# Optimization experiments

Hardware: AMD Instinct MI355X
Metric: run time of the kernel (lower is better)

The kernel has to match this reference:

```python
import jax, jax.numpy as jnp
import numpy as np

N_NODES = 50000
N_EDGES = 1200000
N_REL = 45
IN_C, HID_C, OUT_C = 64, 32, 16


def setup_inputs() -> dict:
    key = jax.random.key(0)
    ks = jax.random.split(key, 9)
    x = jax.random.normal(ks[0], (N_NODES, IN_C), dtype=jnp.float32)
    edge_index = jax.random.randint(ks[1], (2, N_EDGES), 0, N_NODES, dtype=jnp.int64)
    edge_type = jax.random.randint(ks[2], (N_EDGES,), 0, N_REL, dtype=jnp.int64)
    s = 0.05
    W1 = jax.random.normal(ks[3], (N_REL, IN_C, HID_C), dtype=jnp.float32) * s
    root1 = jax.random.normal(ks[4], (IN_C, HID_C), dtype=jnp.float32) * s
    b1 = jax.random.normal(ks[5], (HID_C,), dtype=jnp.float32) * s
    W2 = jax.random.normal(ks[6], (N_REL, HID_C, OUT_C), dtype=jnp.float32) * s
    root2 = jax.random.normal(ks[7], (HID_C, OUT_C), dtype=jnp.float32) * s
    b2 = jax.random.normal(ks[8], (OUT_C,), dtype=jnp.float32) * s
    return {"x": x, "edge_index": edge_index, "edge_type": edge_type,
            "W1": W1, "root1": root1, "b1": b1,
            "W2": W2, "root2": root2, "b2": b2}


def rgcn_conv(x, edge_index, edge_type, W, root, b):
    # PyG RGCNConv: out_i = x_i @ root + b + sum_r mean_{j in N_r(i)} (x_j @ W_r)
    N = x.shape[0]
    R = W.shape[0]
    src, dst = edge_index[0], edge_index[1]
    # per-relation transform of all nodes: [R, N, out]
    h = jnp.einsum('ni,rio->rno', x, W)
    # per-edge message: gather transformed src feature for edge's relation
    msg = h[edge_type, src]                      # [E, out]
    # segment id combines (relation, dst) for per-relation mean aggregation
    seg = edge_type * N + dst                    # [E]
    sums = jax.ops.segment_sum(msg, seg, num_segments=R * N)        # [R*N, out]
    cnt = jax.ops.segment_sum(jnp.ones((msg.shape[0],), x.dtype), seg,
                              num_segments=R * N)                   # [R*N]
    mean = sums / jnp.maximum(cnt, 1.0)[:, None]
    agg = mean.reshape(R, N, -1).sum(axis=0)     # sum over relations -> [N, out]
    return agg + x @ root + b


def reference(x, edge_index, edge_type, W1, root1, b1, W2, root2, b2):
    h = rgcn_conv(x, edge_index, edge_type, W1, root1, b1)
    h = jax.nn.relu(h)
    out = rgcn_conv(h, edge_index, edge_type, W2, root2, b2)
    return out
```

## Files before the change

kernel.cpp:

```cpp
#include <hip/hip_runtime.h>
#include <hip/hip_fp16.h>
#include <cstdint>
#include <cstddef>

#define NN   50000
#define NE   1200000
#define NR   45
#define INC  64
#define HIDC 32
#define OUTC 16
#define MAXE 1202880
#define NCHUNK (MAXE/64)
#define EPB 4096
#define NB  ((NE + EPB - 1) / EPB)
#define QDW2 12500
#define QDD2 25000
#define NTILE ((NN + 255) / 256)


typedef _Float16 f16x8 __attribute__((ext_vector_type(8)));
typedef float    f32x4 __attribute__((ext_vector_type(4)));

union F16Bits { unsigned short u; _Float16 f; };
union ABFrag   { uint4 u; f16x8 f; };

__global__ __launch_bounds__(256) void preph_k(const float* __restrict__ W1,
                                               const float* __restrict__ W2,
                                               const float* __restrict__ x,
                                               const int* __restrict__ ei,
                                               const int* __restrict__ et,
                                               __half* __restrict__ W1f,
                                               __half* __restrict__ W2f,
                                               __half* __restrict__ xh,
                                               unsigned* __restrict__ ghist,
                                               unsigned* __restrict__ rsorted,
                                               unsigned* __restrict__ flagbuf) {
    __shared__ unsigned lh[NR];
    int t = threadIdx.x, b = blockIdx.x;
    if (t < NR) lh[t] = 0;
    __syncthreads();
    if (b < NB) {
        #pragma unroll
        for (int it = 0; it < EPB / 256; ++it) {
            int e = b * EPB + it * 256 + t;
            if (e < NE) {
                int r = et[e], src = ei[e], dst = ei[NE + e];
                if ((unsigned)r < NR && (unsigned)src < NN && (unsigned)dst < NN)
                    atomicAdd(&lh[r], 1u);
            }
        }
    }
    __syncthreads();
    if (b < NB && t < NR) ghist[b * NR + t] = lh[t];
    int g = b * 256 + t;
    int gthreads = gridDim.x * 256;
    for (int i = g; i < MAXE; i += gthreads) rsorted[i] = 0xFFFFFFFFu;
    if (b == 0) flagbuf[t] = 0;
    if (g < NR * 2048) {
        int r = g >> 11, rem = g & 2047;
        int kb = rem >> 10, nb = (rem >> 9) & 1;
        int lane = (rem >> 3) & 63, j = rem & 7;
        int k = kb * 32 + (lane >> 4) * 8 + j;
        int n = nb * 16 + (lane & 15);
        W1f[g] = __float2half(W1[(r * INC + k) * HIDC + n]);
    }
    if (g < NR * 512) {
        int r = g >> 9, rem = g & 511;
        int lane = (rem >> 3) & 63, j = rem & 7;
        int k = (lane >> 4) * 8 + j;
        int kc = (k >> 1) + ((k & 1) << 4);
        int n = lane & 15;
        W2f[g] = __float2half(W2[(r * HIDC + kc) * OUTC + n]);
    }
    if (g < NN * INC / 2) {
        float2 f = ((const float2*)x)[g];
        union { __half2 h; unsigned u; } cv;
        cv.h = __floats2half2_rn(f.x, f.y);
        ((unsigned*)xh)[g] = cv.u;
    }
}

__global__ __launch_bounds__(1024) void scat_k(const int* __restrict__ ei,
                                               const int* __restrict__ et,
                                               const unsigned* __restrict__ ghist,
                                               unsigned* __restrict__ rngs,
                                               int* __restrict__ chunkrel,
                                               unsigned* __restrict__ rsorted) {
    __shared__ unsigned reltot[NR];
    __shared__ unsigned mypart[NR];
    __shared__ unsigned relbase[NR + 1];
    __shared__ unsigned lbase[NR], lcur[NR];
    int t = threadIdx.x, bx = blockIdx.x;
    if (t < NR) {
        unsigned total = 0, part = 0;
        for (int b = 0; b < NB; ++b) {
            if (b == bx) part = total;
            total += ghist[b * NR + t];
        }
        reltot[t] = total;
        mypart[t] = part;
        lcur[t] = 0;
    }
    __syncthreads();
    if (t == 0) {
        unsigned acc = 0;
        for (int r = 0; r < NR; ++r) {
            relbase[r] = acc;
            acc += ((reltot[r] + 63u) >> 6) << 6;
        }
        relbase[NR] = acc;
    }
    __syncthreads();
    if (t < NR) lbase[t] = relbase[t] + mypart[t];
    __syncthreads();
    #pragma unroll
    for (int it = 0; it < EPB / 1024; ++it) {
        int e = bx * EPB + it * 1024 + t;
        if (e < NE) {
            int r = et[e], src = ei[e], dst = ei[NE + e];
            if ((unsigned)r < NR && (unsigned)src < NN && (unsigned)dst < NN) {
                unsigned local = atomicAdd(&lcur[r], 1u);
                rsorted[lbase[r] + local] = (unsigned)src | ((unsigned)dst << 16);
            }
        }
    }
    if (bx == 0) {
        if (t < NR) {
            rngs[2 * t]     = relbase[t];
            rngs[2 * t + 1] = relbase[t] + reltot[t];
        }
        for (int c = t; c < NCHUNK; c += 1024) {
            unsigned pos = (unsigned)c << 6;
            int lo = 0, hi = NR - 1;
            while (lo < hi) {
                int mid = (lo + hi + 1) >> 1;
                if (relbase[mid] <= pos) lo = mid; else hi = mid - 1;
            }
            chunkrel[c] = lo;
        }
    }
}

__global__ __launch_bounds__(1024) void relcnt_k(const unsigned* __restrict__ rsorted,
                                                 const unsigned* __restrict__ rngs,
                                                 unsigned short* __restrict__ cnt16,
                                                 unsigned short* __restrict__ rank16) {
    __shared__ unsigned lds[QDW2];
    int r = blockIdx.x >> 1, q = blockIdx.x & 1, t = threadIdx.x;
    unsigned base = rngs[2 * r], end = rngs[2 * r + 1];
    unsigned dlo = q * QDD2, dhi = dlo + QDD2;
    for (int w = t; w < QDW2; w += 1024) lds[w] = 0;
    __syncthreads();
    for (unsigned s = base + t; s < end; s += 1024) {
        unsigned d = rsorted[s] >> 16;
        if (d >= dlo && d < dhi) {
            unsigned off = d - dlo;
            unsigned old = atomicAdd(&lds[off >> 1], (off & 1) ? 0x10000u : 1u);
            rank16[s] = (unsigned short)((off & 1) ? (old >> 16) : (old & 0xFFFFu));
        }
    }
    __syncthreads();
    unsigned* __restrict__ cp = (unsigned*)(cnt16 + (size_t)r * NN + dlo);
    for (int w = t; w < QDW2; w += 1024) cp[w] = lds[w];
}

__global__ __launch_bounds__(256) void dp_k(const unsigned short* __restrict__ cnt16,
                                            unsigned* __restrict__ packed,
                                            unsigned* __restrict__ rowptr,
                                            unsigned* __restrict__ flags) {
    __shared__ unsigned wsum[4];
    __shared__ unsigned excl_s;
    int t = threadIdx.x, b = blockIdx.x;
    int lane = t & 63, wv = t >> 6;
    int dst = b * 256 + t;
    unsigned deg = 0;
    if (dst < NN) {
        unsigned run = 0;
        #pragma unroll 5
        for (int r = 0; r < NR; ++r) {
            unsigned c = cnt16[(size_t)r * NN + dst];
            F16Bits fb; fb.f = (_Float16)(c ? 1.0f / (float)c : 0.0f);
            packed[(size_t)r * NN + dst] = (run & 0xFFFFu) | ((unsigned)fb.u << 16);
            run += c;
        }
        deg = run;
    }
    unsigned s = deg;
    #pragma unroll
    for (int off = 1; off < 64; off <<= 1) {
        unsigned n = __shfl_up(s, off);
        if (lane >= off) s += n;
    }
    if (lane == 63) wsum[wv] = s;
    __syncthreads();
    unsigned waveoff = 0;
    if (wv > 0) waveoff += wsum[0];
    if (wv > 1) waveoff += wsum[1];
    if (wv > 2) waveoff += wsum[2];
    unsigned blockT = wsum[0] + wsum[1] + wsum[2] + wsum[3];
    unsigned local_excl = waveoff + s - deg;
    if (t == 0) {
        if (b == 0) {
            excl_s = 0;
            atomicExch(&flags[0], 0x80000000u | blockT);
        } else {
            atomicExch(&flags[b], 0x40000000u | blockT);
            unsigned ex = 0;
            int p = b - 1;
            while (p >= 0) {
                unsigned f = atomicAdd(&flags[p], 0u);
                unsigned st = f >> 30;
                if (st == 0) continue;
                ex += f & 0x3FFFFFFFu;
                if (st >= 2) break;
                --p;
            }
            excl_s = ex;
            atomicExch(&flags[b], 0x80000000u | (ex + blockT));
        }
    }
    __syncthreads();
    unsigned ex = excl_s;
    if (dst < NN) rowptr[dst] = ex + local_excl;
    if (b == (int)gridDim.x - 1 && t == 0) rowptr[NN] = ex + blockT;
}

__global__ __launch_bounds__(256) void finalize_k(const unsigned* __restrict__ rsorted,
                                                  const unsigned short* __restrict__ rank16,
                                                  const unsigned* __restrict__ packed,
                                                  const unsigned* __restrict__ rowptr,
                                                  const int* __restrict__ chunkrel,
                                                  uint2* __restrict__ pedges) {
    int s = blockIdx.x * 256 + threadIdx.x;
    if (s >= MAXE) return;
    unsigned v = rsorted[s];
    unsigned dst = v >> 16;
    if (dst >= NN) { pedges[s] = make_uint2(0u, 0x80000000u); return; }
    int r = chunkrel[s >> 6];
    unsigned pk = packed[(size_t)r * NN + dst];
    unsigned dpos = rowptr[dst] + (pk & 0xFFFFu) + (unsigned)rank16[s];
    pedges[s] = make_uint2((v & 0xFFFFu) | (pk & 0xFFFF0000u),
                           dpos | ((unsigned)r << 25));
}

__global__ __launch_bounds__(256) void msg1_k(const __half* __restrict__ xh,
                                              const __half* __restrict__ W1f,
                                              const uint2* __restrict__ pedges,
                                              __half* __restrict__ msg) {
    int tid = threadIdx.x;
    int lane = tid & 63;
    int wave = (blockIdx.x * 256 + tid) >> 6;
    if (wave >= NCHUNK) return;
    int e = (wave << 6) + lane;
    uint2 er = pedges[e];
    int w1 = (int)er.y;
    int rel = __builtin_amdgcn_readfirstlane((w1 >> 25) & 63);
    F16Bits fb; fb.u = (unsigned short)(er.x >> 16);
    float sc = (float)fb.f;
    int src = er.x & 0xFFFF;
    int drow = (w1 < 0) ? NE : (w1 & 0x1FFFFFF);
    const uint4* __restrict__ wf = (const uint4*)W1f + (size_t)rel * 256;
    ABFrag b00, b01, b10, b11;
    b00.u = wf[0 * 64 + lane];
    b01.u = wf[1 * 64 + lane];
    b10.u = wf[2 * 64 + lane];
    b11.u = wf[3 * 64 + lane];
    int quad = lane >> 4, col = lane & 15;
    ABFrag a0[4], a1[4];
    #pragma unroll
    for (int tl = 0; tl < 4; ++tl) {
        int s = __shfl(src, tl * 16 + col);
        const uint4* __restrict__ xp = (const uint4*)(xh + (size_t)s * INC) + quad;
        a0[tl].u = xp[0];
        a1[tl].u = xp[4];
    }
    #pragma unroll
    for (int tl = 0; tl < 4; ++tl) {
        f32x4 acc0 = {0.f, 0.f, 0.f, 0.f}, acc1 = {0.f, 0.f, 0.f, 0.f};
        acc0 = __builtin_amdgcn_mfma_f32_16x16x32_f16(a0[tl].f, b00.f, acc0, 0, 0, 0);
        acc0 = __builtin_amdgcn_mfma_f32_16x16x32_f16(a1[tl].f, b10.f, acc0, 0, 0, 0);
        acc1 = __builtin_amdgcn_mfma_f32_16x16x32_f16(a0[tl].f, b01.f, acc1, 0, 0, 0);
        acc1 = __builtin_amdgcn_mfma_f32_16x16x32_f16(a1[tl].f, b11.f, acc1, 0, 0, 0);
        #pragma unroll
        for (int i = 0; i < 4; ++i) {
            int ee = tl * 16 + quad * 4 + i;
            int dr   = __shfl(drow, ee);
            float si = __shfl(sc, ee);
            union { __half2 h; unsigned u; } cv;
            cv.h = __floats2half2_rn(acc0[i] * si, acc1[i] * si);
            ((unsigned*)(msg + (size_t)dr * HIDC))[col] = cv.u;
        }
    }
}

__global__ __launch_bounds__(256) void msg2_k(const __half* __restrict__ hh,
                                              const __half* __restrict__ W2f,
                                              const uint2* __restrict__ pedges,
                                              __half* __restrict__ msg) {
    int tid = threadIdx.x;
    int lane = tid & 63;
    int wave = (blockIdx.x * 256 + tid) >> 6;
    if (wave >= NCHUNK) return;
    int e = (wave << 6) + lane;
    uint2 er = pedges[e];
    int w1 = (int)er.y;
    int rel = __builtin_amdgcn_readfirstlane((w1 >> 25) & 63);
    F16Bits fb; fb.u = (unsigned short)(er.x >> 16);
    float sc = (float)fb.f;
    int src = er.x & 0xFFFF;
    int drow = (w1 < 0) ? NE : (w1 & 0x1FFFFFF);
    ABFrag bf;
    bf.u = ((const uint4*)W2f + (size_t)rel * 64)[lane];
    int quad = lane >> 4, col = lane & 15;
    ABFrag a[4];
    #pragma unroll
    for (int tl = 0; tl < 4; ++tl) {
        int s = __shfl(src, tl * 16 + col);
        a[tl].u = *((const uint4*)(hh + (size_t)s * HIDC) + quad);
    }
    #pragma unroll
    for (int tl = 0; tl < 4; ++tl) {
        f32x4 acc = {0.f, 0.f, 0.f, 0.f};
        acc = __builtin_amdgcn_mfma_f32_16x16x32_f16(a[tl].f, bf.f, acc, 0, 0, 0);
        #pragma unroll
        for (int i = 0; i < 4; ++i) {
            int ee = tl * 16 + quad * 4 + i;
            int dr   = __shfl(drow, ee);
            float si = __shfl(sc, ee);
            float v  = acc[i] * si;
            float p  = __shfl_xor(v, 8);
            if (col < 8) {
                union { __half2 h; unsigned u; } cv;
                cv.h = __floats2half2_rn(v, p);
                ((unsigned*)(msg + (size_t)dr * OUTC))[col] = cv.u;
            }
        }
    }
}

__global__ __launch_bounds__(256) void gather1_k(const float* __restrict__ x,
                                                 const float* __restrict__ root1,
                                                 const float* __restrict__ b1,
                                                 const __half* __restrict__ msg,
                                                 const unsigned* __restrict__ rowptr,
                                                 __half* __restrict__ hh) {
    __shared__ float sr[INC * HIDC];
    for (int k = threadIdx.x; k < INC * HIDC; k += 256) sr[k] = root1[k];
    __syncthreads();
    int wid = (blockIdx.x * 256 + threadIdx.x) >> 6;
    int lane = threadIdx.x & 63;
    int c2 = lane & 15, sub = lane >> 4;
    unsigned k0 = rowptr[wid], k1 = rowptr[wid + 1];
    float accx = 0.f, accy = 0.f;
    for (unsigned k = k0 + sub; k < k1; k += 4) {
        union { __half2 hh2; unsigned u; } cv;
        cv.u = ((const unsigned*)(msg + (size_t)k * HIDC))[c2];
        float2 f = __half22float2(cv.hh2);
        accx += f.x; accy += f.y;
    }
    const float4* __restrict__ xp = (const float4*)(x + (size_t)wid * INC + sub * 16);
    #pragma unroll
    for (int q = 0; q < 4; ++q) {
        float4 xr = xp[q];
        const float* xs = (const float*)&xr;
        #pragma unroll
        for (int j = 0; j < 4; ++j) {
            int in = sub * 16 + q * 4 + j;
            accx = fmaf(xs[j], sr[in * HIDC + c2], accx);
            accy = fmaf(xs[j], sr[in * HIDC + c2 + 16], accy);
        }
    }
    accx += __shfl_xor(accx, 16); accy += __shfl_xor(accy, 16);
    accx += __shfl_xor(accx, 32); accy += __shfl_xor(accy, 32);
    if (sub == 0) {
        float vx = accx + b1[c2], vy = accy + b1[c2 + 16];
        union { __half2 h2; unsigned u; } cv;
        cv.h2 = __floats2half2_rn(vx > 0.f ? vx : 0.f, vy > 0.f ? vy : 0.f);
        ((unsigned*)hh)[(size_t)wid * (HIDC / 2) + c2] = cv.u;
    }
}

__global__ __launch_bounds__(256) void gather2_k(const __half* __restrict__ hh,
                                                 const float* __restrict__ root2,
                                                 const float* __restrict__ b2,
                                                 const __half* __restrict__ msg,
                                                 const unsigned* __restrict__ rowptr,
                                                 float* __restrict__ out) {
    __shared__ float sr[HIDC * OUTC];
    for (int k = threadIdx.x; k < HIDC * OUTC; k += 256) sr[k] = root2[k];
    __syncthreads();
    int wid = (blockIdx.x * 256 + threadIdx.x) >> 6;
    int lane = threadIdx.x & 63;
    int c2 = lane & 7, sub = lane >> 3;
    unsigned k0 = rowptr[wid], k1 = rowptr[wid + 1];
    float accx = 0.f, accy = 0.f;
    for (unsigned k = k0 + sub; k < k1; k += 8) {
        union { __half2 hh2; unsigned u; } cv;
        cv.u = ((const unsigned*)(msg + (size_t)k * OUTC))[c2];
        float2 f = __half22float2(cv.hh2);
        accx += f.x; accy += f.y;
    }
    uint2 hw = *(const uint2*)(hh + (size_t)wid * HIDC + sub * 4);
    union { __half2 h2; unsigned u; } ca, cb;
    ca.u = hw.x; cb.u = hw.y;
    float2 ha = __half22float2(ca.h2), hb = __half22float2(cb.h2);
    float hs[4] = { ha.x, ha.y, hb.x, hb.y };
    #pragma unroll
    for (int j = 0; j < 4; ++j) {
        int in = 2 * sub + (j >> 1) + ((j & 1) << 4);
        accx = fmaf(hs[j], sr[in * OUTC + c2], accx);
        accy = fmaf(hs[j], sr[in * OUTC + c2 + 8], accy);
    }
    accx += __shfl_xor(accx, 8);  accy += __shfl_xor(accy, 8);
    accx += __shfl_xor(accx, 16); accy += __shfl_xor(accy, 16);
    accx += __shfl_xor(accx, 32); accy += __shfl_xor(accy, 32);
    if (sub == 0) {
        out[(size_t)wid * OUTC + c2]     = accx + b2[c2];
        out[(size_t)wid * OUTC + c2 + 8] = accy + b2[c2 + 8];
    }
}

extern "C" void kernel_launch(void* const* d_in, const int* in_sizes, int n_in,
                              void* d_out, int out_size, void* d_ws, size_t ws_size,
                              hipStream_t stream) {
    const float* x     = (const float*)d_in[0];
    const int*   ei    = (const int*)d_in[1];
    const int*   et    = (const int*)d_in[2];
    const float* W1    = (const float*)d_in[3];
    const float* root1 = (const float*)d_in[4];
    const float* b1    = (const float*)d_in[5];
    const float* W2    = (const float*)d_in[6];
    const float* root2 = (const float*)d_in[7];
    const float* b2    = (const float*)d_in[8];
    float* out = (float*)d_out;

    char* ws = (char*)d_ws;
    size_t o = 0;
    auto alloc = [&](size_t bytes) -> char* {
        char* p = ws + o;
        o = (o + bytes + 255) & ~(size_t)255;
        return p;
    };
    unsigned* rsorted = (unsigned*)alloc((size_t)MAXE * 4);
    unsigned* flagbuf = (unsigned*)alloc(256 * 4);
    unsigned* ghist   = (unsigned*)alloc((size_t)NR * NB * 4);
    unsigned* rngs    = (unsigned*)alloc((size_t)NR * 2 * 4);
    int*      chunkrel= (int*)     alloc((size_t)NCHUNK * 4);
    unsigned short* rank16 = (unsigned short*)alloc((size_t)MAXE * 2);
    unsigned short* cnt16  = (unsigned short*)alloc((size_t)NR * NN * 2);
    unsigned* packed  = (unsigned*)alloc((size_t)NR * NN * 4);
    unsigned* rowptr  = (unsigned*)alloc(((size_t)NN + 1) * 4);
    uint2*    pedges  = (uint2*)   alloc((size_t)MAXE * 8);
    __half*   W1f     = (__half*)  alloc((size_t)NR * 2048 * 2);
    __half*   W2f     = (__half*)  alloc((size_t)NR * 512 * 2);
    __half*   xh      = (__half*)  alloc((size_t)NN * INC * 2);
    __half*   hh      = (__half*)  alloc((size_t)NN * HIDC * 2);
    char*     msgraw  = alloc(((size_t)NE + 1) * 64);
    __half*   msg1    = (__half*)msgraw;
    __half*   msg2    = (__half*)msgraw;

    int prep_grid = NN * INC / 2 / 256;
    preph_k   <<<prep_grid, 256, 0, stream>>>(W1, W2, x, ei, et, W1f, W2f, xh,
                                              ghist, rsorted, flagbuf);
    scat_k    <<<NB, 1024, 0, stream>>>(ei, et, ghist, rngs, chunkrel, rsorted);
    relcnt_k  <<<2 * NR, 1024, 0, stream>>>(rsorted, rngs, cnt16, rank16);
    dp_k      <<<NTILE, 256, 0, stream>>>(cnt16, packed, rowptr, flagbuf + 32);
    finalize_k<<<(MAXE + 255) / 256, 256, 0, stream>>>(rsorted, rank16, packed,
                                                       rowptr, chunkrel, pedges);
    msg1_k    <<<(MAXE + 255) / 256, 256, 0, stream>>>(xh, W1f, pedges, msg1);
    gather1_k <<<NN * 64 / 256, 256, 0, stream>>>(x, root1, b1, msg1, rowptr, hh);
    msg2_k    <<<(MAXE + 255) / 256, 256, 0, stream>>>(hh, W2f, pedges, msg2);
    gather2_k <<<NN * 64 / 256, 256, 0, stream>>>(hh, root2, b2, msg2, rowptr, out);
}
```

Baseline: 296.8 us.

## Privatize histograms, transpose ghist, split relcnt finer, add nontemporal hints, fp16 root input

```diff
diff --git a/kernel.cpp b/kernel.cpp
--- a/kernel.cpp
+++ b/kernel.cpp
@@ -13,8 +13,8 @@
 #define NCHUNK (MAXE/64)
 #define EPB 4096
 #define NB  ((NE + EPB - 1) / EPB)
-#define QDW2 12500
-#define QDD2 25000
+#define QDW 6250
+#define QDD 12500
 #define NTILE ((NN + 255) / 256)
 
 
@@ -35,9 +35,10 @@
                                                unsigned* __restrict__ ghist,
                                                unsigned* __restrict__ rsorted,
                                                unsigned* __restrict__ flagbuf) {
-    __shared__ unsigned lh[NR];
+    __shared__ unsigned lh[4 * 48];
     int t = threadIdx.x, b = blockIdx.x;
-    if (t < NR) lh[t] = 0;
+    int wv = t >> 6;
+    if (t < 192) lh[t] = 0;
     __syncthreads();
     if (b < NB) {
         #pragma unroll
@@ -46,15 +47,17 @@
             if (e < NE) {
                 int r = et[e], src = ei[e], dst = ei[NE + e];
                 if ((unsigned)r < NR && (unsigned)src < NN && (unsigned)dst < NN)
-                    atomicAdd(&lh[r], 1u);
+                    atomicAdd(&lh[wv * 48 + r], 1u);
             }
         }
     }
     __syncthreads();
-    if (b < NB && t < NR) ghist[b * NR + t] = lh[t];
+    if (b < NB && t < NR)
+        ghist[t * NB + b] = lh[t] + lh[48 + t] + lh[96 + t] + lh[144 + t];
     int g = b * 256 + t;
     int gthreads = gridDim.x * 256;
-    for (int i = g; i < MAXE; i += gthreads) rsorted[i] = 0xFFFFFFFFu;
+    for (int i = g; i < MAXE; i += gthreads)
+        __builtin_nontemporal_store(0xFFFFFFFFu, &rsorted[i]);
     if (b == 0) flagbuf[t] = 0;
     if (g < NR * 2048) {
         int r = g >> 11, rem = g & 2047;
@@ -93,9 +96,10 @@
     int t = threadIdx.x, bx = blockIdx.x;
     if (t < NR) {
         unsigned total = 0, part = 0;
+        const unsigned* __restrict__ row = ghist + t * NB;
         for (int b = 0; b < NB; ++b) {
             if (b == bx) part = total;
-            total += ghist[b * NR + t];
+            total += row[b];
         }
         reltot[t] = total;
         mypart[t] = part;
@@ -145,11 +149,11 @@
                                                  const unsigned* __restrict__ rngs,
                                                  unsigned short* __restrict__ cnt16,
                                                  unsigned short* __restrict__ rank16) {
-    __shared__ unsigned lds[QDW2];
-    int r = blockIdx.x >> 1, q = blockIdx.x & 1, t = threadIdx.x;
+    __shared__ unsigned lds[QDW];
+    int r = blockIdx.x >> 2, q = blockIdx.x & 3, t = threadIdx.x;
     unsigned base = rngs[2 * r], end = rngs[2 * r + 1];
-    unsigned dlo = q * QDD2, dhi = dlo + QDD2;
-    for (int w = t; w < QDW2; w += 1024) lds[w] = 0;
+    unsigned dlo = q * QDD, dhi = dlo + QDD;
+    for (int w = t; w < QDW; w += 1024) lds[w] = 0;
     __syncthreads();
     for (unsigned s = base + t; s < end; s += 1024) {
         unsigned d = rsorted[s] >> 16;
@@ -161,7 +165,7 @@
     }
     __syncthreads();
     unsigned* __restrict__ cp = (unsigned*)(cnt16 + (size_t)r * NN + dlo);
-    for (int w = t; w < QDW2; w += 1024) cp[w] = lds[w];
+    for (int w = t; w < QDW; w += 1024) cp[w] = lds[w];
 }
 
 __global__ __launch_bounds__(256) void dp_k(const unsigned short* __restrict__ cnt16,
@@ -233,12 +237,13 @@
                                                   uint2* __restrict__ pedges) {
     int s = blockIdx.x * 256 + threadIdx.x;
     if (s >= MAXE) return;
-    unsigned v = rsorted[s];
+    unsigned v = __builtin_nontemporal_load(&rsorted[s]);
     unsigned dst = v >> 16;
     if (dst >= NN) { pedges[s] = make_uint2(0u, 0x80000000u); return; }
     int r = chunkrel[s >> 6];
     unsigned pk = packed[(size_t)r * NN + dst];
-    unsigned dpos = rowptr[dst] + (pk & 0xFFFFu) + (unsigned)rank16[s];
+    unsigned rk = __builtin_nontemporal_load(&rank16[s]);
+    unsigned dpos = rowptr[dst] + (pk & 0xFFFFu) + rk;
     pedges[s] = make_uint2((v & 0xFFFFu) | (pk & 0xFFFF0000u),
                            dpos | ((unsigned)r << 25));
 }
@@ -288,7 +293,8 @@
             float si = __shfl(sc, ee);
             union { __half2 h; unsigned u; } cv;
             cv.h = __floats2half2_rn(acc0[i] * si, acc1[i] * si);
-            ((unsigned*)(msg + (size_t)dr * HIDC))[col] = cv.u;
+            __builtin_nontemporal_store(cv.u,
+                &((unsigned*)(msg + (size_t)dr * HIDC))[col]);
         }
     }
 }
@@ -332,13 +338,14 @@
             if (col < 8) {
                 union { __half2 h; unsigned u; } cv;
                 cv.h = __floats2half2_rn(v, p);
-                ((unsigned*)(msg + (size_t)dr * OUTC))[col] = cv.u;
+                __builtin_nontemporal_store(cv.u,
+                    &((unsigned*)(msg + (size_t)dr * OUTC))[col]);
             }
         }
     }
 }
 
-__global__ __launch_bounds__(256) void gather1_k(const float* __restrict__ x,
+__global__ __launch_bounds__(256) void gather1_k(const __half* __restrict__ xh,
                                                  const float* __restrict__ root1,
                                                  const float* __restrict__ b1,
                                                  const __half* __restrict__ msg,
@@ -354,21 +361,33 @@
     float accx = 0.f, accy = 0.f;
     for (unsigned k = k0 + sub; k < k1; k += 4) {
         union { __half2 hh2; unsigned u; } cv;
-        cv.u = ((const unsigned*)(msg + (size_t)k * HIDC))[c2];
+        cv.u = __builtin_nontemporal_load(
+            &((const unsigned*)(msg + (size_t)k * HIDC))[c2]);
         float2 f = __half22float2(cv.hh2);
         accx += f.x; accy += f.y;
     }
-    const float4* __restrict__ xp = (const float4*)(x + (size_t)wid * INC + sub * 16);
+    const uint4* __restrict__ xp =
+        (const uint4*)(xh + (size_t)wid * INC + sub * 16);
+    union { uint4 u; __half2 h[4]; } ua, ub;
+    ua.u = xp[0];
+    ub.u = xp[1];
     #pragma unroll
     for (int q = 0; q < 4; ++q) {
-        float4 xr = xp[q];
-        const float* xs = (const float*)&xr;
-        #pragma unroll
-        for (int j = 0; j < 4; ++j) {
-            int in = sub * 16 + q * 4 + j;
-            accx = fmaf(xs[j], sr[in * HIDC + c2], accx);
-            accy = fmaf(xs[j], sr[in * HIDC + c2 + 16], accy);
-        }
+        float2 f = __half22float2(ua.h[q]);
+        int in = sub * 16 + 2 * q;
+        accx = fmaf(f.x, sr[in * HIDC + c2], accx);
+        accy = fmaf(f.x, sr[in * HIDC + c2 + 16], accy);
+        accx = fmaf(f.y, sr[(in + 1) * HIDC + c2], accx);
+        accy = fmaf(f.y, sr[(in + 1) * HIDC + c2 + 16], accy);
+    }
+    #pragma unroll
+    for (int q = 0; q < 4; ++q) {
+        float2 f = __half22float2(ub.h[q]);
+        int in = sub * 16 + 8 + 2 * q;
+        accx = fmaf(f.x, sr[in * HIDC + c2], accx);
+        accy = fmaf(f.x, sr[in * HIDC + c2 + 16], accy);
+        accx = fmaf(f.y, sr[(in + 1) * HIDC + c2], accx);
+        accy = fmaf(f.y, sr[(in + 1) * HIDC + c2 + 16], accy);
     }
     accx += __shfl_xor(accx, 16); accy += __shfl_xor(accy, 16);
     accx += __shfl_xor(accx, 32); accy += __shfl_xor(accy, 32);
@@ -396,7 +415,8 @@
     float accx = 0.f, accy = 0.f;
     for (unsigned k = k0 + sub; k < k1; k += 8) {
         union { __half2 hh2; unsigned u; } cv;
-        cv.u = ((const unsigned*)(msg + (size_t)k * OUTC))[c2];
+        cv.u = __builtin_nontemporal_load(
+            &((const unsigned*)(msg + (size_t)k * OUTC))[c2]);
         float2 f = __half22float2(cv.hh2);
         accx += f.x; accy += f.y;
     }
@@ -463,12 +483,12 @@
     preph_k   <<<prep_grid, 256, 0, stream>>>(W1, W2, x, ei, et, W1f, W2f, xh,
                                               ghist, rsorted, flagbuf);
     scat_k    <<<NB, 1024, 0, stream>>>(ei, et, ghist, rngs, chunkrel, rsorted);
-    relcnt_k  <<<2 * NR, 1024, 0, stream>>>(rsorted, rngs, cnt16, rank16);
+    relcnt_k  <<<4 * NR, 1024, 0, stream>>>(rsorted, rngs, cnt16, rank16);
     dp_k      <<<NTILE, 256, 0, stream>>>(cnt16, packed, rowptr, flagbuf + 32);
     finalize_k<<<(MAXE + 255) / 256, 256, 0, stream>>>(rsorted, rank16, packed,
                                                        rowptr, chunkrel, pedges);
     msg1_k    <<<(MAXE + 255) / 256, 256, 0, stream>>>(xh, W1f, pedges, msg1);
-    gather1_k <<<NN * 64 / 256, 256, 0, stream>>>(x, root1, b1, msg1, rowptr, hh);
+    gather1_k <<<NN * 64 / 256, 256, 0, stream>>>(xh, root1, b1, msg1, rowptr, hh);
     msg2_k    <<<(MAXE + 255) / 256, 256, 0, stream>>>(hh, W2f, pedges, msg2);
     gather2_k <<<NN * 64 / 256, 256, 0, stream>>>(hh, root2, b2, msg2, rowptr, out);
 }
```

Result: slower. 375.0 us (+26.3%).
